# Kernel optimization log

Hardware: AMD Instinct MI355X
Metric: run time of the kernel (lower is better)

The kernel has to match this reference:

```python
import jax, jax.numpy as jnp
import numpy as np

ALPHA, BETA, GAMMA, DELTA = 0.3, 0.3, 0.2, 0.2
BK, BW = 3, 3.0
EPS = 1e-7


def _bce_with_logits(x, y):
    # numerically stable: max(x,0) - x*y + log(1+exp(-|x|)); pos_weight=1.0
    return jnp.maximum(x, 0.0) - x * y + jnp.log1p(jnp.exp(-jnp.abs(x)))


def _lovasz_hinge_flat(x, y):
    # x, y: (N,) flattened logits / binary labels for one image
    signs = 2.0 * y - 1.0
    errors = 1.0 - x * signs
    perm = jnp.argsort(-errors)            # descending sort permutation
    errors_sorted = errors[perm]
    gt_sorted = y[perm]
    gts = gt_sorted.sum()
    intersection = gts - jnp.cumsum(gt_sorted)
    union = gts + jnp.cumsum(1.0 - gt_sorted)
    jaccard = 1.0 - intersection / union
    jaccard = jnp.concatenate([jaccard[:1], jaccard[1:] - jaccard[:-1]])
    return jnp.dot(jax.nn.relu(errors_sorted), jaccard)


def setup_inputs() -> dict:
    key = jax.random.key(0)
    k1, k2 = jax.random.split(key)
    logits = jax.random.normal(k1, (32, 1, 512, 512), dtype=jnp.float32)
    # binary ground-truth mask (0/1 floats)
    targets = jnp.round(jax.random.uniform(k2, (32, 1, 512, 512), dtype=jnp.float32))
    return {"logits": logits, "targets": targets}


def reference(logits, targets):
    # --- BCE term (pos_weight = 1.0) ---
    bce_elem = _bce_with_logits(logits, targets)
    bce = bce_elem.mean()

    # --- Dice term ---
    probs = jax.nn.sigmoid(logits)
    num = 2.0 * (probs * targets).sum(axis=(2, 3))
    den = (probs + targets).sum(axis=(2, 3)) + EPS
    dice = 1.0 - (num / den).mean()

    # --- Boundary-weighted BCE term (weights computed under no_grad) ---
    kernel = jnp.ones((1, 1, BK, BK), logits.dtype) / (BK * BK)
    smooth = jax.lax.conv_general_dilated(
        targets, kernel, window_strides=(1, 1), padding='SAME',
        dimension_numbers=('NCHW', 'OIHW', 'NCHW'))
    edges = ((smooth > 0.01) & (smooth < 0.99)).astype(logits.dtype)
    weights = jax.lax.stop_gradient(1.0 + edges * (BW - 1.0))
    boundary = (bce_elem * weights).mean()

    # --- Lovasz hinge, per image then averaged ---
    B = logits.shape[0]
    lov = jax.vmap(_lovasz_hinge_flat)(
        logits.reshape(B, -1), targets.reshape(B, -1)).mean()

    return ALPHA * bce + BETA * dice + GAMMA * boundary + DELTA * lov
```

## Files before the change

### kernel.cpp

```cpp
#include <hip/hip_runtime.h>
#include <hip/hip_bf16.h>


#define NB      32
#define HH      512
#define WW      512
#define HW      (HH*WW)
#define NTOT    (NB*HW)
#define K_BINS  1024
#define INV_H   128.0f
#define BIN_W   (1.0f/128.0f)
#define BPI     16

struct Ws {
    unsigned cnt[NB*BPI*K_BINS];
    float    partf[NB*BPI*5];
    float4   vals[NB];
    unsigned ticket;
};

__device__ __forceinline__ void process_elem(float x, float y, float wsum,
                                             float& bce_s, float& bceE_s, float& sy_s,
                                             float& spy_s, float& P_s,
                                             unsigned* s_cnt) {
    const float ax = fabsf(x);
    const float t  = __expf(-ax);
    const float bce = fmaxf(x, 0.f) - x * y + __logf(1.f + t);
    const float inv = __builtin_amdgcn_rcpf(1.f + t);
    const float s = (x >= 0.f) ? inv : t * inv;
    const bool edge = (wsum > 0.5f) && (wsum < 8.5f);

    bce_s  += bce;
    bceE_s += edge ? bce : 0.f;
    sy_s   += s * y;
    spy_s  += s + y;
    P_s    += y;

    const float e = 1.f - x * (2.f * y - 1.f);
    if (e > 0.f) {
        int b = (int)(e * INV_H);
        if (b > K_BINS - 1) b = K_BINS - 1;
        atomicAdd(&s_cnt[b], (y > 0.5f) ? 0x10001u : 1u);
    }
}

__global__ __launch_bounds__(256, 2) void kernelA(const float* __restrict__ logits,
                                                  const float* __restrict__ targets,
                                                  Ws* __restrict__ ws) {
    __shared__ unsigned s_cnt[K_BINS];
    __shared__ float    red[4][5];

    const int tid  = threadIdx.x;
    const int lane = tid & 63;
    const int wave = tid >> 6;
    for (int i = tid; i < K_BINS; i += 256) s_cnt[i] = 0u;
    __syncthreads();

    const int img   = blockIdx.x >> 4;
    const int strip = ((blockIdx.x & 15) << 2) | wave;
    const int r0    = strip * 8;

    const float4* __restrict__ tg4 = (const float4*)(targets + img * HW);
    const float4* __restrict__ lg4 = (const float4*)(logits  + img * HW);
    const int cA = lane;
    const int cB = 64 + lane;

    float4 T[5][2]; float fT[5];
    float4 X[3][2];

#pragma unroll
    for (int s = 0; s < 5; ++s) {
        const int rr = r0 - 1 + s;
        const int rc = rr < 0 ? 0 : (rr > 511 ? 511 : rr);
        fT[s] = (rr >= 0 && rr < 512) ? 1.f : 0.f;
        T[s][0] = tg4[rc * 128 + cA];
        T[s][1] = tg4[rc * 128 + cB];
    }
#pragma unroll
    for (int s = 0; s < 3; ++s) {
        const int rr = r0 + s;
        X[s][0] = lg4[rr * 128 + cA];
        X[s][1] = lg4[rr * 128 + cB];
    }

    float bce_s = 0.f, bceE_s = 0.f, sy_s = 0.f, spy_s = 0.f, P_s = 0.f;

#pragma unroll
    for (int j = 0; j < 8; ++j) {
        const int ia = j % 5, ib = (j + 1) % 5, ic = (j + 2) % 5;
        const int xs = j % 3;
        const float fa = fT[ia], fc = fT[ic];

        float4 csA, csB;
        csA.x = fmaf(T[ia][0].x, fa, fmaf(T[ic][0].x, fc, T[ib][0].x));
        csA.y = fmaf(T[ia][0].y, fa, fmaf(T[ic][0].y, fc, T[ib][0].y));
        csA.z = fmaf(T[ia][0].z, fa, fmaf(T[ic][0].z, fc, T[ib][0].z));
        csA.w = fmaf(T[ia][0].w, fa, fmaf(T[ic][0].w, fc, T[ib][0].w));
        csB.x = fmaf(T[ia][1].x, fa, fmaf(T[ic][1].x, fc, T[ib][1].x));
        csB.y = fmaf(T[ia][1].y, fa, fmaf(T[ic][1].y, fc, T[ib][1].y));
        csB.z = fmaf(T[ia][1].z, fa, fmaf(T[ic][1].z, fc, T[ib][1].z));
        csB.w = fmaf(T[ia][1].w, fa, fmaf(T[ic][1].w, fc, T[ib][1].w));

        const float upA  = __shfl_up(csA.w, 1);
        const float dnA  = __shfl_down(csA.x, 1);
        const float upB  = __shfl_up(csB.w, 1);
        const float dnB  = __shfl_down(csB.x, 1);
        const float bc0  = __shfl(csB.x, 0);
        const float bc63 = __shfl(csA.w, 63);
        const float LA = (lane == 0)  ? 0.f  : upA;
        const float RA = (lane == 63) ? bc0  : dnA;
        const float LB = (lane == 0)  ? bc63 : upB;
        const float RB = (lane == 63) ? 0.f  : dnB;

        process_elem(X[xs][0].x, T[ib][0].x, LA + csA.x + csA.y,    bce_s, bceE_s, sy_s, spy_s, P_s, s_cnt);
        process_elem(X[xs][0].y, T[ib][0].y, csA.x + csA.y + csA.z, bce_s, bceE_s, sy_s, spy_s, P_s, s_cnt);
        process_elem(X[xs][0].z, T[ib][0].z, csA.y + csA.z + csA.w, bce_s, bceE_s, sy_s, spy_s, P_s, s_cnt);
        process_elem(X[xs][0].w, T[ib][0].w, csA.z + csA.w + RA,    bce_s, bceE_s, sy_s, spy_s, P_s, s_cnt);
        process_elem(X[xs][1].x, T[ib][1].x, LB + csB.x + csB.y,    bce_s, bceE_s, sy_s, spy_s, P_s, s_cnt);
        process_elem(X[xs][1].y, T[ib][1].y, csB.x + csB.y + csB.z, bce_s, bceE_s, sy_s, spy_s, P_s, s_cnt);
        process_elem(X[xs][1].z, T[ib][1].z, csB.y + csB.z + csB.w, bce_s, bceE_s, sy_s, spy_s, P_s, s_cnt);
        process_elem(X[xs][1].w, T[ib][1].w, csB.z + csB.w + RB,    bce_s, bceE_s, sy_s, spy_s, P_s, s_cnt);

        if (j < 5) {
            const int rr = r0 + j + 4;
            const int rc = rr > 511 ? 511 : rr;
            fT[ia] = (rr < 512) ? 1.f : 0.f;
            T[ia][0] = tg4[rc * 128 + cA];
            T[ia][1] = tg4[rc * 128 + cB];
            const int rx = r0 + j + 3;
            X[xs][0] = lg4[rx * 128 + cA];
            X[xs][1] = lg4[rx * 128 + cB];
        }
    }
    __syncthreads();

    unsigned* g_c = ws->cnt + blockIdx.x * K_BINS;
    for (int i = tid; i < K_BINS; i += 256) g_c[i] = s_cnt[i];

    for (int off = 32; off; off >>= 1) {
        bce_s  += __shfl_down(bce_s, off);
        bceE_s += __shfl_down(bceE_s, off);
        sy_s   += __shfl_down(sy_s, off);
        spy_s  += __shfl_down(spy_s, off);
        P_s    += __shfl_down(P_s, off);
    }
    if (lane == 0) {
        red[wave][0] = bce_s; red[wave][1] = bceE_s; red[wave][2] = sy_s;
        red[wave][3] = spy_s; red[wave][4] = P_s;
    }
    __syncthreads();
    if (tid == 0) {
        float a = 0.f, b = 0.f, c2 = 0.f, d = 0.f, e2 = 0.f;
        for (int w = 0; w < 4; ++w) {
            a += red[w][0]; b += red[w][1]; c2 += red[w][2];
            d += red[w][3]; e2 += red[w][4];
        }
        float* pf = ws->partf + blockIdx.x * 5;
        pf[0] = a; pf[1] = b; pf[2] = c2; pf[3] = d; pf[4] = e2;
        if (blockIdx.x == 0) ws->ticket = 0u;
    }
}

__global__ __launch_bounds__(256) void kernelBC(Ws* __restrict__ ws,
                                                float* __restrict__ out) {
    __shared__ unsigned sc_a[256];
    __shared__ unsigned sc_p[256];
    __shared__ double   dred[4];
    __shared__ float    s_P, s_bce, s_bceE, s_dice;
    __shared__ int      s_last;

    const int img = blockIdx.x;
    const int tid = threadIdx.x;

    float pf0 = 0.f, pf1 = 0.f, pf2 = 0.f, pf3 = 0.f, pf4 = 0.f;
    if (tid < BPI) {
        const float* p = ws->partf + (img * BPI + tid) * 5;
        pf0 = p[0]; pf1 = p[1]; pf2 = p[2]; pf3 = p[3]; pf4 = p[4];
    }
    if (tid < 64) {
        for (int off = 8; off; off >>= 1) {
            pf0 += __shfl_down(pf0, off);
            pf1 += __shfl_down(pf1, off);
            pf2 += __shfl_down(pf2, off);
            pf3 += __shfl_down(pf3, off);
            pf4 += __shfl_down(pf4, off);
        }
        if (tid == 0) {
            s_bce  = pf0;
            s_bceE = pf1;
            s_dice = 2.f * pf2 / (pf3 + 1e-7f);
            s_P    = pf4;
        }
    }
    __syncthreads();

    const unsigned* __restrict__ cn = ws->cnt + img * BPI * K_BINS;
    unsigned la[4], lp[4];
    float    me[4];
    unsigned tot_a = 0, tot_p = 0;
#pragma unroll
    for (int j = 0; j < 4; ++j) {
        const int k = K_BINS - 1 - (tid * 4 + j);
        unsigned a = 0, p = 0;
#pragma unroll
        for (int b = 0; b < BPI; ++b) {
            const unsigned cpk = cn[b * K_BINS + k];
            a += cpk & 0xFFFFu;
            p += cpk >> 16;
        }
        la[j] = a; lp[j] = p;
        me[j] = ((float)k + 0.5f) * BIN_W;
        tot_a += a; tot_p += p;
    }

    sc_a[tid] = tot_a; sc_p[tid] = tot_p;
    __syncthreads();
    for (int off = 1; off < 256; off <<= 1) {
        unsigned va = (tid >= off) ? sc_a[tid - off] : 0u;
        unsigned vp = (tid >= off) ? sc_p[tid - off] : 0u;
        __syncthreads();
        sc_a[tid] += va; sc_p[tid] += vp;
        __syncthreads();
    }
    const unsigned excl_a = sc_a[tid] - tot_a;
    const unsigned excl_p = sc_p[tid] - tot_p;

    const double P = (double)s_P;
    double run_a = (double)excl_a, run_p = (double)excl_p;
    double contrib = 0.0;
#pragma unroll
    for (int j = 0; j < 4; ++j) {
        const double m = (double)la[j];
        const double p = (double)lp[j];
        if (la[j]) {
            const double u = P + (run_a + 0.5 * m) - (run_p + 0.5 * p);
            const double c = run_p + 0.5 * p;
            contrib += (double)(lp[j] * me[j]) / u;
            const double den = u * (u - 1.0);
            if (den > 0.0)
                contrib += (double)((la[j] - lp[j]) * me[j]) * (P - c) / den;
        }
        run_a += m; run_p += p;
    }

    for (int off = 32; off; off >>= 1) contrib += __shfl_down(contrib, off);
    const int wave = tid >> 6;
    const int lane = tid & 63;
    if (lane == 0) dred[wave] = contrib;
    __syncthreads();

    if (tid == 0) {
        const double tot = dred[0] + dred[1] + dred[2] + dred[3];
        float4 v;
        v.x = s_bce; v.y = s_bceE; v.z = s_dice; v.w = (float)tot;
        ws->vals[img] = v;
        __threadfence();
        const unsigned old = atomicAdd(&ws->ticket, 1u);
        s_last = (old == NB - 1) ? 1 : 0;
    }
    __syncthreads();

    if (s_last) {
        __threadfence();
        if (tid < 64) {
            float vx = 0.f, vy = 0.f, vz = 0.f, vw = 0.f;
            if (tid < NB) {
                const float4 v = ws->vals[tid];
                vx = v.x; vy = v.y; vz = v.z; vw = v.w;
            }
            for (int off = 16; off; off >>= 1) {
                vx += __shfl_down(vx, off);
                vy += __shfl_down(vy, off);
                vz += __shfl_down(vz, off);
                vw += __shfl_down(vw, off);
            }
            if (tid == 0) {
                const float invN = 1.f / (float)NTOT;
                const float bce      = vx * invN;
                const float boundary = (vx + 2.f * vy) * invN;
                const float dice     = 1.f - vz / (float)NB;
                const float lov      = vw / (float)NB;
                out[0] = 0.3f * bce + 0.3f * dice + 0.2f * boundary + 0.2f * lov;
            }
        }
    }
}

extern "C" void kernel_launch(void* const* d_in, const int* in_sizes, int n_in,
                              void* d_out, int out_size, void* d_ws, size_t ws_size,
                              hipStream_t stream) {
    const float* logits  = (const float*)d_in[0];
    const float* targets = (const float*)d_in[1];
    float* out = (float*)d_out;
    Ws* ws = (Ws*)d_ws;

    kernelA<<<NB * BPI, 256, 0, stream>>>(logits, targets, ws);
    kernelBC<<<NB, 256, 0, stream>>>(ws, out);
}
```

Before: 108.0 us.

## Fuse per-image Lovasz reduction into histogram kernel via last-block tickets

```diff
diff --git a/kernel.cpp b/kernel.cpp
--- a/kernel.cpp
+++ b/kernel.cpp
@@ -10,13 +10,15 @@
 #define K_BINS  1024
 #define INV_H   128.0f
 #define BIN_W   (1.0f/128.0f)
-#define BPI     16
+#define ROWS    4
+#define BPI     32
 
 struct Ws {
+    unsigned tick[NB];
+    unsigned gticket;
     unsigned cnt[NB*BPI*K_BINS];
     float    partf[NB*BPI*5];
     float4   vals[NB];
-    unsigned ticket;
 };
 
 __device__ __forceinline__ void process_elem(float x, float y, float wsum,
@@ -44,11 +46,15 @@
     }
 }
 
-__global__ __launch_bounds__(256, 2) void kernelA(const float* __restrict__ logits,
+__global__ __launch_bounds__(256, 4) void kernelA(const float* __restrict__ logits,
                                                   const float* __restrict__ targets,
-                                                  Ws* __restrict__ ws) {
+                                                  Ws* __restrict__ ws,
+                                                  float* __restrict__ out) {
     __shared__ unsigned s_cnt[K_BINS];
     __shared__ float    red[4][5];
+    __shared__ double   dred[4];
+    __shared__ float    s_P, s_bce, s_bceE, s_dice;
+    __shared__ int      s_last, s_fin;
 
     const int tid  = threadIdx.x;
     const int lane = tid & 63;
@@ -56,9 +62,9 @@
     for (int i = tid; i < K_BINS; i += 256) s_cnt[i] = 0u;
     __syncthreads();
 
-    const int img   = blockIdx.x >> 4;
-    const int strip = ((blockIdx.x & 15) << 2) | wave;
-    const int r0    = strip * 8;
+    const int img   = blockIdx.x >> 5;
+    const int strip = ((blockIdx.x & 31) << 2) | wave;
+    const int r0    = strip * ROWS;
 
     const float4* __restrict__ tg4 = (const float4*)(targets + img * HW);
     const float4* __restrict__ lg4 = (const float4*)(logits  + img * HW);
@@ -86,7 +92,7 @@
     float bce_s = 0.f, bceE_s = 0.f, sy_s = 0.f, spy_s = 0.f, P_s = 0.f;
 
 #pragma unroll
-    for (int j = 0; j < 8; ++j) {
+    for (int j = 0; j < ROWS; ++j) {
         const int ia = j % 5, ib = (j + 1) % 5, ic = (j + 2) % 5;
         const int xs = j % 3;
         const float fa = fT[ia], fc = fT[ic];
@@ -121,7 +127,7 @@
         process_elem(X[xs][1].z, T[ib][1].z, csB.y + csB.z + csB.w, bce_s, bceE_s, sy_s, spy_s, P_s, s_cnt);
         process_elem(X[xs][1].w, T[ib][1].w, csB.z + csB.w + RB,    bce_s, bceE_s, sy_s, spy_s, P_s, s_cnt);
 
-        if (j < 5) {
+        if (j < ROWS - 3) {
             const int rr = r0 + j + 4;
             const int rc = rr > 511 ? 511 : rr;
             fT[ia] = (rr < 512) ? 1.f : 0.f;
@@ -157,20 +163,14 @@
         }
         float* pf = ws->partf + blockIdx.x * 5;
         pf[0] = a; pf[1] = b; pf[2] = c2; pf[3] = d; pf[4] = e2;
-        if (blockIdx.x == 0) ws->ticket = 0u;
-    }
-}
-
-__global__ __launch_bounds__(256) void kernelBC(Ws* __restrict__ ws,
-                                                float* __restrict__ out) {
-    __shared__ unsigned sc_a[256];
-    __shared__ unsigned sc_p[256];
-    __shared__ double   dred[4];
-    __shared__ float    s_P, s_bce, s_bceE, s_dice;
-    __shared__ int      s_last;
-
-    const int img = blockIdx.x;
-    const int tid = threadIdx.x;
+        __threadfence();
+        const unsigned old = atomicAdd(&ws->tick[img], 1u);
+        s_last = (old == BPI - 1) ? 1 : 0;
+    }
+    __syncthreads();
+    if (!s_last) return;
+
+    __threadfence();
 
     float pf0 = 0.f, pf1 = 0.f, pf2 = 0.f, pf3 = 0.f, pf4 = 0.f;
     if (tid < BPI) {
@@ -178,7 +178,7 @@
         pf0 = p[0]; pf1 = p[1]; pf2 = p[2]; pf3 = p[3]; pf4 = p[4];
     }
     if (tid < 64) {
-        for (int off = 8; off; off >>= 1) {
+        for (int off = 16; off; off >>= 1) {
             pf0 += __shfl_down(pf0, off);
             pf1 += __shfl_down(pf1, off);
             pf2 += __shfl_down(pf2, off);
@@ -192,7 +192,6 @@
             s_P    = pf4;
         }
     }
-    __syncthreads();
 
     const unsigned* __restrict__ cn = ws->cnt + img * BPI * K_BINS;
     unsigned la[4], lp[4];
@@ -213,6 +212,8 @@
         tot_a += a; tot_p += p;
     }
 
+    unsigned* sc_a = s_cnt;
+    unsigned* sc_p = s_cnt + 256;
     sc_a[tid] = tot_a; sc_p[tid] = tot_p;
     __syncthreads();
     for (int off = 1; off < 256; off <<= 1) {
@@ -244,8 +245,6 @@
     }
 
     for (int off = 32; off; off >>= 1) contrib += __shfl_down(contrib, off);
-    const int wave = tid >> 6;
-    const int lane = tid & 63;
     if (lane == 0) dred[wave] = contrib;
     __syncthreads();
 
@@ -255,33 +254,32 @@
         v.x = s_bce; v.y = s_bceE; v.z = s_dice; v.w = (float)tot;
         ws->vals[img] = v;
         __threadfence();
-        const unsigned old = atomicAdd(&ws->ticket, 1u);
-        s_last = (old == NB - 1) ? 1 : 0;
-    }
-    __syncthreads();
-
-    if (s_last) {
-        __threadfence();
-        if (tid < 64) {
-            float vx = 0.f, vy = 0.f, vz = 0.f, vw = 0.f;
-            if (tid < NB) {
-                const float4 v = ws->vals[tid];
-                vx = v.x; vy = v.y; vz = v.z; vw = v.w;
-            }
-            for (int off = 16; off; off >>= 1) {
-                vx += __shfl_down(vx, off);
-                vy += __shfl_down(vy, off);
-                vz += __shfl_down(vz, off);
-                vw += __shfl_down(vw, off);
-            }
-            if (tid == 0) {
-                const float invN = 1.f / (float)NTOT;
-                const float bce      = vx * invN;
-                const float boundary = (vx + 2.f * vy) * invN;
-                const float dice     = 1.f - vz / (float)NB;
-                const float lov      = vw / (float)NB;
-                out[0] = 0.3f * bce + 0.3f * dice + 0.2f * boundary + 0.2f * lov;
-            }
+        const unsigned gold = atomicAdd(&ws->gticket, 1u);
+        s_fin = (gold == NB - 1) ? 1 : 0;
+    }
+    __syncthreads();
+    if (!s_fin) return;
+
+    __threadfence();
+    if (tid < 64) {
+        float vx = 0.f, vy = 0.f, vz = 0.f, vw = 0.f;
+        if (tid < NB) {
+            const float4 v = ws->vals[tid];
+            vx = v.x; vy = v.y; vz = v.z; vw = v.w;
+        }
+        for (int off = 16; off; off >>= 1) {
+            vx += __shfl_down(vx, off);
+            vy += __shfl_down(vy, off);
+            vz += __shfl_down(vz, off);
+            vw += __shfl_down(vw, off);
+        }
+        if (tid == 0) {
+            const float invN = 1.f / (float)NTOT;
+            const float bce      = vx * invN;
+            const float boundary = (vx + 2.f * vy) * invN;
+            const float dice     = 1.f - vz / (float)NB;
+            const float lov      = vw / (float)NB;
+            out[0] = 0.3f * bce + 0.3f * dice + 0.2f * boundary + 0.2f * lov;
         }
     }
 }
@@ -294,6 +292,6 @@
     float* out = (float*)d_out;
     Ws* ws = (Ws*)d_ws;
 
-    kernelA<<<NB * BPI, 256, 0, stream>>>(logits, targets, ws);
-    kernelBC<<<NB, 256, 0, stream>>>(ws, out);
+    (void)hipMemsetAsync(d_ws, 0, (NB + 1) * sizeof(unsigned), stream);
+    kernelA<<<NB * BPI, 256, 0, stream>>>(logits, targets, ws, out);
 }
```

After: 149.4 us. 38.3% more time.

## Halve rows per wave, double blocks per image, and relax cross-block ticket sync

Applied to the files above, without the earlier changes.

```diff
diff --git a/kernel.cpp b/kernel.cpp
--- a/kernel.cpp
+++ b/kernel.cpp
@@ -10,13 +10,16 @@
 #define K_BINS  1024
 #define INV_H   128.0f
 #define BIN_W   (1.0f/128.0f)
-#define BPI     16
+#define ROWS    4
+#define BPI     32
+
+#define AGENT   __HIP_MEMORY_SCOPE_AGENT
 
 struct Ws {
+    unsigned ticket;
     unsigned cnt[NB*BPI*K_BINS];
     float    partf[NB*BPI*5];
-    float4   vals[NB];
-    unsigned ticket;
+    float    vals[NB*4];
 };
 
 __device__ __forceinline__ void process_elem(float x, float y, float wsum,
@@ -44,7 +47,7 @@
     }
 }
 
-__global__ __launch_bounds__(256, 2) void kernelA(const float* __restrict__ logits,
+__global__ __launch_bounds__(256, 4) void kernelA(const float* __restrict__ logits,
                                                   const float* __restrict__ targets,
                                                   Ws* __restrict__ ws) {
     __shared__ unsigned s_cnt[K_BINS];
@@ -56,9 +59,9 @@
     for (int i = tid; i < K_BINS; i += 256) s_cnt[i] = 0u;
     __syncthreads();
 
-    const int img   = blockIdx.x >> 4;
-    const int strip = ((blockIdx.x & 15) << 2) | wave;
-    const int r0    = strip * 8;
+    const int img   = blockIdx.x >> 5;
+    const int strip = ((blockIdx.x & 31) << 2) | wave;
+    const int r0    = strip * ROWS;
 
     const float4* __restrict__ tg4 = (const float4*)(targets + img * HW);
     const float4* __restrict__ lg4 = (const float4*)(logits  + img * HW);
@@ -86,7 +89,7 @@
     float bce_s = 0.f, bceE_s = 0.f, sy_s = 0.f, spy_s = 0.f, P_s = 0.f;
 
 #pragma unroll
-    for (int j = 0; j < 8; ++j) {
+    for (int j = 0; j < ROWS; ++j) {
         const int ia = j % 5, ib = (j + 1) % 5, ic = (j + 2) % 5;
         const int xs = j % 3;
         const float fa = fT[ia], fc = fT[ic];
@@ -121,7 +124,7 @@
         process_elem(X[xs][1].z, T[ib][1].z, csB.y + csB.z + csB.w, bce_s, bceE_s, sy_s, spy_s, P_s, s_cnt);
         process_elem(X[xs][1].w, T[ib][1].w, csB.z + csB.w + RB,    bce_s, bceE_s, sy_s, spy_s, P_s, s_cnt);
 
-        if (j < 5) {
+        if (j < ROWS - 3) {
             const int rr = r0 + j + 4;
             const int rc = rr > 511 ? 511 : rr;
             fT[ia] = (rr < 512) ? 1.f : 0.f;
@@ -178,7 +181,7 @@
         pf0 = p[0]; pf1 = p[1]; pf2 = p[2]; pf3 = p[3]; pf4 = p[4];
     }
     if (tid < 64) {
-        for (int off = 8; off; off >>= 1) {
+        for (int off = 16; off; off >>= 1) {
             pf0 += __shfl_down(pf0, off);
             pf1 += __shfl_down(pf1, off);
             pf2 += __shfl_down(pf2, off);
@@ -251,22 +254,27 @@
 
     if (tid == 0) {
         const double tot = dred[0] + dred[1] + dred[2] + dred[3];
-        float4 v;
-        v.x = s_bce; v.y = s_bceE; v.z = s_dice; v.w = (float)tot;
-        ws->vals[img] = v;
-        __threadfence();
-        const unsigned old = atomicAdd(&ws->ticket, 1u);
+        float* vv = ws->vals + img * 4;
+        __hip_atomic_store(&vv[0], s_bce,      __ATOMIC_RELAXED, AGENT);
+        __hip_atomic_store(&vv[1], s_bceE,     __ATOMIC_RELAXED, AGENT);
+        __hip_atomic_store(&vv[2], s_dice,     __ATOMIC_RELAXED, AGENT);
+        __hip_atomic_store(&vv[3], (float)tot, __ATOMIC_RELAXED, AGENT);
+        asm volatile("s_waitcnt vmcnt(0)" ::: "memory");
+        const unsigned old = __hip_atomic_fetch_add(&ws->ticket, 1u,
+                                                    __ATOMIC_RELAXED, AGENT);
         s_last = (old == NB - 1) ? 1 : 0;
     }
     __syncthreads();
 
     if (s_last) {
-        __threadfence();
         if (tid < 64) {
             float vx = 0.f, vy = 0.f, vz = 0.f, vw = 0.f;
             if (tid < NB) {
-                const float4 v = ws->vals[tid];
-                vx = v.x; vy = v.y; vz = v.z; vw = v.w;
+                const float* vv = ws->vals + tid * 4;
+                vx = __hip_atomic_load(&vv[0], __ATOMIC_RELAXED, AGENT);
+                vy = __hip_atomic_load(&vv[1], __ATOMIC_RELAXED, AGENT);
+                vz = __hip_atomic_load(&vv[2], __ATOMIC_RELAXED, AGENT);
+                vw = __hip_atomic_load(&vv[3], __ATOMIC_RELAXED, AGENT);
             }
             for (int off = 16; off; off >>= 1) {
                 vx += __shfl_down(vx, off);
```

Result: no change. 107.5 us (-0.4%).
